# Kernel optimization log

Hardware: AMD Instinct MI355X
Metric: run time of the kernel (lower is better)

## Reference

```python
import jax, jax.numpy as jnp
import numpy as np

PATCH_SIZES = [4, 8, 16]
B, S, D, H = 32, 1000, 64, 512


def setup_inputs() -> dict:
    key = jax.random.key(0)
    ks = jax.random.split(key, 8)
    inp = {"x": jax.random.normal(ks[0], (B, S, D), dtype=jnp.float32)}
    for i, p in enumerate(PATCH_SIZES):
        fan_in = p * D
        inp[f"W{i}"] = jax.random.normal(ks[1 + 2 * i], (H, fan_in), dtype=jnp.float32) / np.sqrt(fan_in).astype(np.float32)
        inp[f"b{i}"] = jax.random.normal(ks[2 + 2 * i], (H,), dtype=jnp.float32) * 0.01
    inp["pos"] = jax.random.normal(ks[7], (1, 1000, H), dtype=jnp.float32)
    return inp


def reference(x, W0, b0, W1, b1, W2, b2, pos):
    Ws = [W0, W1, W2]
    bs = [b0, b1, b2]
    batch, seq_len, d = x.shape
    min_len = seq_len - max(PATCH_SIZES) + 1  # all scales truncated to this
    embs = []
    for p, W, b in zip(PATCH_SIZES, Ws, bs):
        # sliding windows, stride 1, only the first min_len windows are kept
        idx = jnp.arange(min_len)[:, None] + jnp.arange(p)[None, :]  # (min_len, p)
        win = x[:, idx, :]  # (batch, min_len, p, d) -- im2col gather
        # torch Linear on flattened [time, feature] patch: W[h, t*d + f]
        Wk = W.reshape(-1, p, d)  # (H, p, d)
        embs.append(jnp.einsum('blpd,hpd->blh', win, Wk) + b)
    out = jnp.stack(embs, axis=1).mean(axis=1)  # mean over scales
    return out + pos[:, :min_len, :]
```

## Files before the change

### kernel.cpp

```cpp
#include <hip/hip_runtime.h>
#include <stdint.h>

typedef unsigned short u16;
typedef __attribute__((ext_vector_type(8))) short bf16x8;
typedef __attribute__((ext_vector_type(8))) u16  u16x8;
typedef __attribute__((ext_vector_type(4))) float f32x4;

static constexpr int BATCH  = 32;
static constexpr int SEQ    = 1000;
static constexpr int DIM    = 64;
static constexpr int HOUT   = 512;
static constexpr int MINLEN = 985;
static constexpr int KTOT   = 1024;
static constexpr int AROWS  = 144;

static constexpr size_t XB_OFF   = 0;
static constexpr size_t WF_OFF   = 4u << 20;
static constexpr size_t BE_OFF   = 5u << 20;
static constexpr int    XB_TOTAL = 2048000 + 4096;

__device__ inline u16 f2bf(float f) {
  union { float f; uint32_t u; } v; v.f = f;
  uint32_t r = v.u + 0x7fffu + ((v.u >> 16) & 1u);
  return (u16)(r >> 16);
}

__global__ void pe_prep(const float* __restrict__ x,
                        const float* __restrict__ W0, const float* __restrict__ W1,
                        const float* __restrict__ W2, const float* __restrict__ b0,
                        const float* __restrict__ b1, const float* __restrict__ b2,
                        u16* __restrict__ xb, u16* __restrict__ Wp,
                        float* __restrict__ beff) {
  int bid = blockIdx.x;
  if (bid < 1002) {
    int i = (bid * 256 + threadIdx.x) * 8;
    u16x8 o;
    if (i < 2048000) {
      const float4* p = (const float4*)(x + i);
      float4 a = p[0], c = p[1];
      o[0] = f2bf(a.x); o[1] = f2bf(a.y); o[2] = f2bf(a.z); o[3] = f2bf(a.w);
      o[4] = f2bf(c.x); o[5] = f2bf(c.y); o[6] = f2bf(c.z); o[7] = f2bf(c.w);
    } else {
      o = (u16x8)(0);
    }
    *(u16x8*)(xb + i) = o;
  } else if (bid < 1258) {
    int j  = (bid - 1002) * 256 + threadIdx.x;
    int h  = j >> 7;
    int kc = j & 127;
    float v[8];
    const float4* w2 = (const float4*)(W2 + h * 1024 + kc * 8);
    float4 a = w2[0], c = w2[1];
    v[0]=a.x; v[1]=a.y; v[2]=a.z; v[3]=a.w; v[4]=c.x; v[5]=c.y; v[6]=c.z; v[7]=c.w;
    if (kc < 64) {
      const float4* w1 = (const float4*)(W1 + h * 512 + kc * 8);
      float4 d = w1[0], e = w1[1];
      v[0]+=d.x; v[1]+=d.y; v[2]+=d.z; v[3]+=d.w; v[4]+=e.x; v[5]+=e.y; v[6]+=e.z; v[7]+=e.w;
    }
    if (kc < 32) {
      const float4* w0 = (const float4*)(W0 + h * 256 + kc * 8);
      float4 d = w0[0], e = w0[1];
      v[0]+=d.x; v[1]+=d.y; v[2]+=d.z; v[3]+=d.w; v[4]+=e.x; v[5]+=e.y; v[6]+=e.z; v[7]+=e.w;
    }
    u16x8 o;
    #pragma unroll
    for (int e = 0; e < 8; ++e) o[e] = f2bf(v[e] * (1.0f / 3.0f));
    size_t dst = ((size_t)(h >> 4) * 32 + (kc >> 2)) * 512 + (kc & 3) * 128 + (h & 15) * 8;
    *(u16x8*)(Wp + dst) = o;
  } else {
    int h = (bid - 1258) * 256 + threadIdx.x;
    if (h < HOUT) beff[h] = (b0[h] + b1[h] + b2[h]) * (1.0f / 3.0f);
  }
}

__device__ inline void gload_lds16(const void* g, void* l) {
  __builtin_amdgcn_global_load_lds(
      (const __attribute__((address_space(1))) uint32_t*)g,
      (__attribute__((address_space(3))) uint32_t*)l, 16, 0, 0);
}

__global__ __launch_bounds__(256, 4) void pe_gemm(
    const u16* __restrict__ xb, const u16* __restrict__ Wp,
    const float* __restrict__ beff, const float* __restrict__ pos,
    float* __restrict__ out) {
  __shared__ u16 ldsA[AROWS * 64];

  const int t    = threadIdx.x;
  const int w    = t >> 6;
  const int lane = t & 63;
  const int b    = blockIdx.z;
  const int l0   = blockIdx.y * 128;
  const int n0   = blockIdx.x * 128;
  const int wr   = w >> 1;
  const int wc   = w & 1;
  const int lr   = lane & 15;
  const int g    = lane >> 4;

  const int sra = lane >> 3;
  const int sca = ((lane & 7) ^ sra) * 8;

  const u16* Ab = xb + b * (SEQ * DIM) + l0 * 64;
  const u16* Bp = Wp + ((size_t)((n0 >> 4) + wc * 4) * 32) * 512 + lane * 8;

  #pragma unroll
  for (int i = 0; i < 4; ++i) {
    int c = w * 4 + i;
    gload_lds16(Ab + (c * 8 + sra) * 64 + sca, &ldsA[c * 512]);
  }
  if (w < 2) {
    int c = 16 + w;
    gload_lds16(Ab + (c * 8 + sra) * 64 + sca, &ldsA[c * 512]);
  }

  bf16x8 bA[4], bB[4];
  #pragma unroll
  for (int n = 0; n < 4; ++n)
    bA[n] = *(const bf16x8*)(Bp + (size_t)(n * 32) * 512);

  __syncthreads();

  f32x4 acc[4][4] = {};
  const int rbase = wr * 64 + lr;

  #define A_READS(kt_, aF_)                                                   \
    _Pragma("unroll")                                                         \
    for (int m = 0; m < 4; ++m) {                                             \
      int r = rbase + m * 16 + ((kt_) >> 1);                                  \
      int s = ((((kt_) & 1) << 2) + g) ^ (r & 7);                             \
      aF_[m] = *(const bf16x8*)&ldsA[r * 64 + s * 8];                         \
    }
  #define B_LOADS(kt_, dst_)                                                  \
    _Pragma("unroll")                                                         \
    for (int n = 0; n < 4; ++n)                                               \
      dst_[n] = *(const bf16x8*)(Bp + (size_t)(n * 32 + (kt_)) * 512);
  #define MFMAS(aF_, bF_)                                                     \
    _Pragma("unroll")                                                         \
    for (int m = 0; m < 4; ++m)                                               \
      _Pragma("unroll")                                                       \
      for (int n = 0; n < 4; ++n)                                             \
        acc[m][n] = __builtin_amdgcn_mfma_f32_16x16x32_bf16(aF_[m], bF_[n],   \
                                                            acc[m][n], 0, 0, 0);

  for (int kt = 0; kt < 32; kt += 2) {
    bf16x8 aF[4];
    if (kt + 1 < 32) { B_LOADS(kt + 1, bB); }
    A_READS(kt, aF);
    MFMAS(aF, bA);
    if (kt + 2 < 32) { B_LOADS(kt + 2, bA); }
    A_READS(kt + 1, aF);
    MFMAS(aF, bB);
  }
  #undef A_READS
  #undef B_LOADS
  #undef MFMAS

  #pragma unroll
  for (int n = 0; n < 4; ++n) {
    const int h  = n0 + wc * 64 + n * 16 + lr;
    const float bv = beff[h];
    #pragma unroll
    for (int m = 0; m < 4; ++m) {
      const int rowb = l0 + wr * 64 + m * 16 + (g << 2);
      #pragma unroll
      for (int r = 0; r < 4; ++r) {
        const int l = rowb + r;
        if (l < MINLEN) {
          out[((size_t)b * MINLEN + l) * HOUT + h] =
              acc[m][n][r] + bv + pos[(size_t)l * HOUT + h];
        }
      }
    }
  }
}

extern "C" void kernel_launch(void* const* d_in, const int* in_sizes, int n_in,
                              void* d_out, int out_size, void* d_ws, size_t ws_size,
                              hipStream_t stream) {
  const float* x   = (const float*)d_in[0];
  const float* W0  = (const float*)d_in[1];
  const float* b0  = (const float*)d_in[2];
  const float* W1  = (const float*)d_in[3];
  const float* b1  = (const float*)d_in[4];
  const float* W2  = (const float*)d_in[5];
  const float* b2  = (const float*)d_in[6];
  const float* pos = (const float*)d_in[7];
  float* out = (float*)d_out;

  char* ws  = (char*)d_ws;
  u16*  xbf = (u16*)(ws + XB_OFF);
  u16*  Wp  = (u16*)(ws + WF_OFF);
  float* be = (float*)(ws + BE_OFF);

  hipLaunchKernelGGL(pe_prep, dim3(1260), dim3(256), 0, stream,
                     x, W0, W1, W2, b0, b1, b2, xbf, Wp, be);
  hipLaunchKernelGGL(pe_gemm, dim3(HOUT / 128, 8, BATCH), dim3(256), 0, stream,
                     xbf, Wp, be, pos, out);
}
```

Measured before the change: 54.79 us.

## Fuse x bf16 conversion into GEMM and double M tile per block

Removes the separate x-to-bf16 pass in the prep kernel. The GEMM now reads fp32 x directly, converts it and writes it swizzled into LDS. The M tile per block doubles from 128 to 256 rows (8x4 accumulators per wave, occupancy hint lowered to 2), which halves the number of B-weight reloads per row. MFMA sections are also wrapped in s_setprio. In exchange, the LDS fill becomes a synchronous register round-trip instead of async global_load_lds, register pressure rises, and boundary blocks waste more work since 985 rows do not divide evenly into 256-row tiles.

```diff
diff --git a/kernel.cpp b/kernel.cpp
--- a/kernel.cpp
+++ b/kernel.cpp
@@ -11,13 +11,10 @@
 static constexpr int DIM    = 64;
 static constexpr int HOUT   = 512;
 static constexpr int MINLEN = 985;
-static constexpr int KTOT   = 1024;
-static constexpr int AROWS  = 144;
+static constexpr int AROWS  = 272;
 
-static constexpr size_t XB_OFF   = 0;
-static constexpr size_t WF_OFF   = 4u << 20;
-static constexpr size_t BE_OFF   = 5u << 20;
-static constexpr int    XB_TOTAL = 2048000 + 4096;
+static constexpr size_t WF_OFF = 4u << 20;
+static constexpr size_t BE_OFF = 5u << 20;
 
 __device__ inline u16 f2bf(float f) {
   union { float f; uint32_t u; } v; v.f = f;
@@ -25,27 +22,13 @@
   return (u16)(r >> 16);
 }
 
-__global__ void pe_prep(const float* __restrict__ x,
-                        const float* __restrict__ W0, const float* __restrict__ W1,
+__global__ void pe_prep(const float* __restrict__ W0, const float* __restrict__ W1,
                         const float* __restrict__ W2, const float* __restrict__ b0,
                         const float* __restrict__ b1, const float* __restrict__ b2,
-                        u16* __restrict__ xb, u16* __restrict__ Wp,
-                        float* __restrict__ beff) {
+                        u16* __restrict__ Wp, float* __restrict__ beff) {
   int bid = blockIdx.x;
-  if (bid < 1002) {
-    int i = (bid * 256 + threadIdx.x) * 8;
-    u16x8 o;
-    if (i < 2048000) {
-      const float4* p = (const float4*)(x + i);
-      float4 a = p[0], c = p[1];
-      o[0] = f2bf(a.x); o[1] = f2bf(a.y); o[2] = f2bf(a.z); o[3] = f2bf(a.w);
-      o[4] = f2bf(c.x); o[5] = f2bf(c.y); o[6] = f2bf(c.z); o[7] = f2bf(c.w);
-    } else {
-      o = (u16x8)(0);
-    }
-    *(u16x8*)(xb + i) = o;
-  } else if (bid < 1258) {
-    int j  = (bid - 1002) * 256 + threadIdx.x;
+  if (bid < 256) {
+    int j  = bid * 256 + threadIdx.x;
     int h  = j >> 7;
     int kc = j & 127;
     float v[8];
@@ -68,19 +51,13 @@
     size_t dst = ((size_t)(h >> 4) * 32 + (kc >> 2)) * 512 + (kc & 3) * 128 + (h & 15) * 8;
     *(u16x8*)(Wp + dst) = o;
   } else {
-    int h = (bid - 1258) * 256 + threadIdx.x;
+    int h = (bid - 256) * 256 + threadIdx.x;
     if (h < HOUT) beff[h] = (b0[h] + b1[h] + b2[h]) * (1.0f / 3.0f);
   }
 }
 
-__device__ inline void gload_lds16(const void* g, void* l) {
-  __builtin_amdgcn_global_load_lds(
-      (const __attribute__((address_space(1))) uint32_t*)g,
-      (__attribute__((address_space(3))) uint32_t*)l, 16, 0, 0);
-}
-
-__global__ __launch_bounds__(256, 4) void pe_gemm(
-    const u16* __restrict__ xb, const u16* __restrict__ Wp,
+__global__ __launch_bounds__(256, 2) void pe_gemm(
+    const float* __restrict__ x, const u16* __restrict__ Wp,
     const float* __restrict__ beff, const float* __restrict__ pos,
     float* __restrict__ out) {
   __shared__ u16 ldsA[AROWS * 64];
@@ -89,27 +66,32 @@
   const int w    = t >> 6;
   const int lane = t & 63;
   const int b    = blockIdx.z;
-  const int l0   = blockIdx.y * 128;
+  const int l0   = blockIdx.y * 256;
   const int n0   = blockIdx.x * 128;
   const int wr   = w >> 1;
   const int wc   = w & 1;
   const int lr   = lane & 15;
   const int g    = lane >> 4;
 
-  const int sra = lane >> 3;
-  const int sca = ((lane & 7) ^ sra) * 8;
-
-  const u16* Ab = xb + b * (SEQ * DIM) + l0 * 64;
   const u16* Bp = Wp + ((size_t)((n0 >> 4) + wc * 4) * 32) * 512 + lane * 8;
 
-  #pragma unroll
-  for (int i = 0; i < 4; ++i) {
-    int c = w * 4 + i;
-    gload_lds16(Ab + (c * 8 + sra) * 64 + sca, &ldsA[c * 512]);
-  }
-  if (w < 2) {
-    int c = 16 + w;
-    gload_lds16(Ab + (c * 8 + sra) * 64 + sca, &ldsA[c * 512]);
+  const float* Ax = x + (size_t)b * (SEQ * DIM) + l0 * 64;
+  for (int it = 0; it < 9; ++it) {
+    int idx = it * 256 + t;
+    if (idx < AROWS * 8) {
+      int row = idx >> 3, ch = idx & 7;
+      u16x8 o;
+      if (l0 + row < SEQ) {
+        const float4* p = (const float4*)(Ax + row * 64 + ch * 8);
+        float4 a = p[0], c = p[1];
+        o[0] = f2bf(a.x); o[1] = f2bf(a.y); o[2] = f2bf(a.z); o[3] = f2bf(a.w);
+        o[4] = f2bf(c.x); o[5] = f2bf(c.y); o[6] = f2bf(c.z); o[7] = f2bf(c.w);
+      } else {
+        o = (u16x8)(0);
+      }
+      int s = ch ^ (row & 7);
+      *(u16x8*)&ldsA[row * 64 + s * 8] = o;
+    }
   }
 
   bf16x8 bA[4], bB[4];
@@ -119,12 +101,12 @@
 
   __syncthreads();
 
-  f32x4 acc[4][4] = {};
-  const int rbase = wr * 64 + lr;
+  f32x4 acc[8][4] = {};
+  const int rbase = wr * 128 + lr;
 
   #define A_READS(kt_, aF_)                                                   \
     _Pragma("unroll")                                                         \
-    for (int m = 0; m < 4; ++m) {                                             \
+    for (int m = 0; m < 8; ++m) {                                             \
       int r = rbase + m * 16 + ((kt_) >> 1);                                  \
       int s = ((((kt_) & 1) << 2) + g) ^ (r & 7);                             \
       aF_[m] = *(const bf16x8*)&ldsA[r * 64 + s * 8];                         \
@@ -134,15 +116,17 @@
     for (int n = 0; n < 4; ++n)                                               \
       dst_[n] = *(const bf16x8*)(Bp + (size_t)(n * 32 + (kt_)) * 512);
   #define MFMAS(aF_, bF_)                                                     \
+    __builtin_amdgcn_s_setprio(1);                                            \
     _Pragma("unroll")                                                         \
-    for (int m = 0; m < 4; ++m)                                               \
+    for (int m = 0; m < 8; ++m)                                               \
       _Pragma("unroll")                                                       \
       for (int n = 0; n < 4; ++n)                                             \
         acc[m][n] = __builtin_amdgcn_mfma_f32_16x16x32_bf16(aF_[m], bF_[n],   \
-                                                            acc[m][n], 0, 0, 0);
+                                                            acc[m][n], 0, 0, 0); \
+    __builtin_amdgcn_s_setprio(0);
 
   for (int kt = 0; kt < 32; kt += 2) {
-    bf16x8 aF[4];
+    bf16x8 aF[8];
     if (kt + 1 < 32) { B_LOADS(kt + 1, bB); }
     A_READS(kt, aF);
     MFMAS(aF, bA);
@@ -159,8 +143,8 @@
     const int h  = n0 + wc * 64 + n * 16 + lr;
     const float bv = beff[h];
     #pragma unroll
-    for (int m = 0; m < 4; ++m) {
-      const int rowb = l0 + wr * 64 + m * 16 + (g << 2);
+    for (int m = 0; m < 8; ++m) {
+      const int rowb = l0 + wr * 128 + m * 16 + (g << 2);
       #pragma unroll
       for (int r = 0; r < 4; ++r) {
         const int l = rowb + r;
@@ -187,12 +171,11 @@
   float* out = (float*)d_out;
 
   char* ws  = (char*)d_ws;
-  u16*  xbf = (u16*)(ws + XB_OFF);
   u16*  Wp  = (u16*)(ws + WF_OFF);
   float* be = (float*)(ws + BE_OFF);
 
-  hipLaunchKernelGGL(pe_prep, dim3(1260), dim3(256), 0, stream,
-                     x, W0, W1, W2, b0, b1, b2, xbf, Wp, be);
-  hipLaunchKernelGGL(pe_gemm, dim3(HOUT / 128, 8, BATCH), dim3(256), 0, stream,
-                     xbf, Wp, be, pos, out);
+  hipLaunchKernelGGL(pe_prep, dim3(258), dim3(256), 0, stream,
+                     W0, W1, W2, b0, b1, b2, Wp, be);
+  hipLaunchKernelGGL(pe_gemm, dim3(HOUT / 128, 4, BATCH), dim3(256), 0, stream,
+                     x, Wp, be, pos, out);
 }
```

Result: slower. 65.63 us (+19.8%).
